# Optimization experiments

Hardware: AMD Instinct MI355X
Metric: run time of the kernel (lower is better)

## Reference

```python
import jax, jax.numpy as jnp
import numpy as np

B, N = 32, 256
PHI1, PHI2 = 64, 128
RHO1, RHO2, OUT = 256, 128, 64


def setup_inputs() -> dict:
    key = jax.random.key(0)
    ks = jax.random.split(key, 12)
    dm = jax.random.normal(ks[0], (B, N, N), dtype=jnp.float32)
    lengths = jnp.clip(jax.random.randint(ks[1], (B,), 0, N), 2, N).astype(jnp.int32)

    def lin(k, fan_in, fan_out):
        # torch nn.Linear default init: U(-1/sqrt(fan_in), 1/sqrt(fan_in))
        bound = 1.0 / np.sqrt(fan_in)
        kw, kb = jax.random.split(k)
        W = jax.random.uniform(kw, (fan_in, fan_out), jnp.float32, -bound, bound)
        b = jax.random.uniform(kb, (fan_out,), jnp.float32, -bound, bound)
        return W, b

    W1, b1 = lin(ks[2], 1, PHI1)
    W2, b2 = lin(ks[3], PHI1, PHI2)
    W3, b3 = lin(ks[4], PHI2, RHO1)
    W4, b4 = lin(ks[5], RHO1, RHO2)
    W5, b5 = lin(ks[6], RHO2, OUT)
    return {"dm": dm, "lengths": lengths, "W1": W1, "b1": b1, "W2": W2, "b2": b2,
            "W3": W3, "b3": b3, "W4": W4, "b4": b4, "W5": W5, "b5": b5}


def reference(dm, lengths, W1, b1, W2, b2, W3, b3, W4, b4, W5, b5):
    # Static upper-triangular (offset=1) index pairs: P = N*(N-1)/2
    iu0, iu1 = jnp.triu_indices(N, k=1)
    scalars = dm[:, iu0, iu1]                                   # [B, P]
    # Ragged mask: a pair (i, j) exists only if both indices < item length
    mask = (iu0[None, :] < lengths[:, None]) & (iu1[None, :] < lengths[:, None])  # [B, P]
    # phi MLP applied per scalar: 1 -> 64 -> 128, ReLU after each
    h = jax.nn.relu(scalars[..., None] * W1[0] + b1)            # [B, P, 64]
    h = jax.nn.relu(jnp.einsum('bpd,de->bpe', h, W2) + b2)      # [B, P, 128]
    # Masked sum-pool over pairs
    pooled = jnp.sum(h * mask[..., None].astype(h.dtype), axis=1)  # [B, 128]
    # rho MLP: 128 -> 256 -> 128 -> OUT (ReLU on hidden layers only)
    r = jax.nn.relu(pooled @ W3 + b3)
    r = jax.nn.relu(r @ W4 + b4)
    return r @ W5 + b5                                           # [B, OUT]
```

## Files before the change

### kernel.cpp

```cpp
#include <hip/hip_runtime.h>
#include <hip/hip_bf16.h>


#define NB 32
#define NN 256
#define PHI2 128
#define SEGS 65

__global__ __launch_bounds__(128) void build_tables(
    const float* __restrict__ W1, const float* __restrict__ b1,
    const float* __restrict__ W2, const float* __restrict__ b2,
    float2* __restrict__ table2,
    float* __restrict__ tsort, float* __restrict__ pooled) {
  __shared__ float w2_s[64 * PHI2];
  __shared__ float t_s[64], w1_s[64], b1_s[64];
  __shared__ int cat_s[64], rank_s[64];
  const int tid = threadIdx.x;
  const int seg = blockIdx.x;
  const float4* W2v = (const float4*)W2;
  float4* w2v = (float4*)w2_s;
  for (int i = tid; i < 64 * PHI2 / 4; i += 128) w2v[i] = W2v[i];
  if (tid < 64) {
    float w = W1[tid], bb = b1[tid];
    w1_s[tid] = w; b1_s[tid] = bb;
    int cat; float t;
    if (w > 0.f)      { cat = 0; t = -bb / w; }
    else if (w < 0.f) { cat = 1; t = -bb / w; }
    else              { cat = (bb > 0.f) ? 2 : 3; t = 0.f; }
    t_s[tid] = t; cat_s[tid] = cat;
  }
  __syncthreads();
  if (tid < 64) {
    float t = t_s[tid]; int r = 0;
    for (int k = 0; k < 64; ++k) {
      float tk = t_s[k];
      r += (tk < t) || (tk == t && k < tid);
    }
    rank_s[tid] = r;
    if (seg == 0) tsort[r] = t;
  }
  __syncthreads();
  float a = 0.f, bsum = b2[tid];
#pragma unroll 8
  for (int j = 0; j < 64; ++j) {
    int cat = cat_s[j], r = rank_s[j];
    bool act = (cat == 0) ? (seg > r) : (cat == 1) ? (seg <= r) : (cat == 2);
    float w2 = w2_s[j * PHI2 + tid];
    float m = act ? 1.f : 0.f;
    a    = fmaf(m * w1_s[j], w2, a);
    bsum = fmaf(m * b1_s[j], w2, bsum);
  }
  table2[seg * PHI2 + tid] = make_float2(a, bsum);
  if (seg == 0) {
    for (int i = tid; i < NB * PHI2; i += 128) pooled[i] = 0.f;
  }
}

__global__ __launch_bounds__(256) void phi_pool(
    const float* __restrict__ dm, const int* __restrict__ lengths,
    const float2* __restrict__ table2, const float* __restrict__ tsort,
    float* __restrict__ pooled) {
  __shared__ float2 ab_s[SEGS * PHI2];
  __shared__ float red_s[4][PHI2];
  const int chunk = blockIdx.x;
  const int b     = blockIdx.y;
  const int tid = threadIdx.x;
  const int lane = tid & 63, w = tid >> 6;

  const int len = lengths[b];
  if (chunk * 4 >= len - 1) return;

  for (int i = tid; i < SEGS * PHI2; i += 256) ab_s[i] = table2[i];
  __syncthreads();

  const float tv = tsort[lane];
  const float* dmb = dm + (size_t)b * (NN * NN);
  float acc0 = 0.f, acc1 = 0.f;

  for (int i0 = chunk * 4 + w; i0 < len - 1; i0 += 128) {
    const float* row = dmb + i0 * NN + i0 + 1;
    const int cnt_total = len - 1 - i0;
    for (int base = 0; base < cnt_total; base += 64) {
      const int cnt = min(64, cnt_total - base);
      float sv = (lane < cnt) ? row[base + lane] : 0.f;
      if (cnt == 64) {
#pragma unroll 8
        for (int j = 0; j < 64; ++j) {
          float s = __int_as_float(__builtin_amdgcn_readlane(__float_as_int(sv), j));
          int pos = (int)__popcll(__ballot(tv < s));
          const float2* rowp = ab_s + pos * PHI2;
          float2 p0 = rowp[lane];
          float2 p1 = rowp[64 + lane];
          acc0 += fmaxf(fmaf(p0.x, s, p0.y), 0.f);
          acc1 += fmaxf(fmaf(p1.x, s, p1.y), 0.f);
        }
      } else {
        for (int j = 0; j < cnt; ++j) {
          float s = __int_as_float(__builtin_amdgcn_readlane(__float_as_int(sv), j));
          int pos = (int)__popcll(__ballot(tv < s));
          const float2* rowp = ab_s + pos * PHI2;
          float2 p0 = rowp[lane];
          float2 p1 = rowp[64 + lane];
          acc0 += fmaxf(fmaf(p0.x, s, p0.y), 0.f);
          acc1 += fmaxf(fmaf(p1.x, s, p1.y), 0.f);
        }
      }
    }
  }
  red_s[w][lane] = acc0;
  red_s[w][64 + lane] = acc1;
  __syncthreads();
  if (tid < PHI2) {
    float v = red_s[0][tid] + red_s[1][tid] + red_s[2][tid] + red_s[3][tid];
    atomicAdd(&pooled[b * PHI2 + tid], v);
  }
}

__global__ __launch_bounds__(256) void rho_mlp(
    const float* __restrict__ pooled,
    const float* __restrict__ W3, const float* __restrict__ b3,
    const float* __restrict__ W4, const float* __restrict__ b4,
    const float* __restrict__ W5, const float* __restrict__ b5,
    float* __restrict__ out) {
  __shared__ float w_s[128 * 256];
  __shared__ float p_s[128], r1_s[256], r2_s[128];
  const int b = blockIdx.x, tid = threadIdx.x;
  float4* wsv = (float4*)w_s;
  {
    const float4* w3v = (const float4*)W3;
    for (int i = tid; i < 8192; i += 256) wsv[i] = w3v[i];
  }
  if (tid < 128) p_s[tid] = pooled[b * 128 + tid];
  __syncthreads();
  {
    float acc = b3[tid];
#pragma unroll 8
    for (int k = 0; k < 128; ++k) acc = fmaf(p_s[k], w_s[k * 256 + tid], acc);
    r1_s[tid] = fmaxf(acc, 0.f);
  }
  __syncthreads();
  {
    const float4* w4v = (const float4*)W4;
    for (int i = tid; i < 8192; i += 256) wsv[i] = w4v[i];
  }
  __syncthreads();
  if (tid < 128) {
    float acc = b4[tid];
#pragma unroll 8
    for (int k = 0; k < 256; ++k) acc = fmaf(r1_s[k], w_s[k * 128 + tid], acc);
    r2_s[tid] = fmaxf(acc, 0.f);
  }
  __syncthreads();
  {
    const float4* w5v = (const float4*)W5;
    for (int i = tid; i < 2048; i += 256) wsv[i] = w5v[i];
  }
  __syncthreads();
  if (tid < 64) {
    float acc = b5[tid];
#pragma unroll 8
    for (int k = 0; k < 128; ++k) acc = fmaf(r2_s[k], w_s[k * 64 + tid], acc);
    out[b * 64 + tid] = acc;
  }
}

extern "C" void kernel_launch(void* const* d_in, const int* in_sizes, int n_in,
                              void* d_out, int out_size, void* d_ws, size_t ws_size,
                              hipStream_t stream) {
  const float* dm      = (const float*)d_in[0];
  const int*   lengths = (const int*)d_in[1];
  const float* W1 = (const float*)d_in[2];
  const float* b1 = (const float*)d_in[3];
  const float* W2 = (const float*)d_in[4];
  const float* b2 = (const float*)d_in[5];
  const float* W3 = (const float*)d_in[6];
  const float* b3 = (const float*)d_in[7];
  const float* W4 = (const float*)d_in[8];
  const float* b4 = (const float*)d_in[9];
  const float* W5 = (const float*)d_in[10];
  const float* b5 = (const float*)d_in[11];

  float* ws = (float*)d_ws;
  float2* table2 = (float2*)ws;
  float* tsort   = ws + 16640;
  float* pooled  = ws + 16704;

  build_tables<<<SEGS, 128, 0, stream>>>(W1, b1, W2, b2, table2, tsort, pooled);
  phi_pool<<<dim3(32, NB), 256, 0, stream>>>(dm, lengths, table2, tsort, pooled);
  rho_mlp<<<NB, 256, 0, stream>>>(pooled, W3, b3, W4, b4, W5, b5, (float*)d_out);
}
```

Measured before the change: 157.4 us.

## Interleave phi table as float4, prefetch rows, use 512-thread blocks with direct atomics

The build_tables kernel now writes each segment's coefficients as float4 (a,b for channels lane and lane+64), so phi_pool fetches both channels with one 16-byte LDS read per pair instead of two float2 reads. phi_pool also loads the next 64-element chunk of the distance row before processing the current one, to hide global latency. Blocks grow to 8 waves (half as many chunks), which halves the per-block table copies into LDS. The shared-memory reduction is replaced by per-wave atomicAdds, which raises atomic traffic to pooled.

```diff
diff --git a/kernel.cpp b/kernel.cpp
--- a/kernel.cpp
+++ b/kernel.cpp
@@ -10,10 +10,11 @@
 __global__ __launch_bounds__(128) void build_tables(
     const float* __restrict__ W1, const float* __restrict__ b1,
     const float* __restrict__ W2, const float* __restrict__ b2,
-    float2* __restrict__ table2,
+    float4* __restrict__ table4,
     float* __restrict__ tsort, float* __restrict__ pooled) {
   __shared__ float w2_s[64 * PHI2];
   __shared__ float t_s[64], w1_s[64], b1_s[64];
+  __shared__ float a_sh[128], b_sh[128];
   __shared__ int cat_s[64], rank_s[64];
   const int tid = threadIdx.x;
   const int seg = blockIdx.x;
@@ -50,70 +51,68 @@
     a    = fmaf(m * w1_s[j], w2, a);
     bsum = fmaf(m * b1_s[j], w2, bsum);
   }
-  table2[seg * PHI2 + tid] = make_float2(a, bsum);
+  a_sh[tid] = a; b_sh[tid] = bsum;
+  __syncthreads();
+  if (tid < 64)
+    table4[seg * 64 + tid] =
+        make_float4(a_sh[tid], b_sh[tid], a_sh[tid + 64], b_sh[tid + 64]);
   if (seg == 0) {
     for (int i = tid; i < NB * PHI2; i += 128) pooled[i] = 0.f;
   }
 }
 
-__global__ __launch_bounds__(256) void phi_pool(
+__global__ __launch_bounds__(512) void phi_pool(
     const float* __restrict__ dm, const int* __restrict__ lengths,
-    const float2* __restrict__ table2, const float* __restrict__ tsort,
+    const float4* __restrict__ table4, const float* __restrict__ tsort,
     float* __restrict__ pooled) {
-  __shared__ float2 ab_s[SEGS * PHI2];
-  __shared__ float red_s[4][PHI2];
+  __shared__ float4 ab_s[SEGS * 64];
   const int chunk = blockIdx.x;
   const int b     = blockIdx.y;
   const int tid = threadIdx.x;
   const int lane = tid & 63, w = tid >> 6;
 
   const int len = lengths[b];
-  if (chunk * 4 >= len - 1) return;
+  if (chunk * 8 >= len - 1) return;
 
-  for (int i = tid; i < SEGS * PHI2; i += 256) ab_s[i] = table2[i];
+  for (int i = tid; i < SEGS * 64; i += 512) ab_s[i] = table4[i];
   __syncthreads();
 
   const float tv = tsort[lane];
   const float* dmb = dm + (size_t)b * (NN * NN);
   float acc0 = 0.f, acc1 = 0.f;
 
-  for (int i0 = chunk * 4 + w; i0 < len - 1; i0 += 128) {
+  for (int i0 = chunk * 8 + w; i0 < len - 1; i0 += 128) {
     const float* row = dmb + i0 * NN + i0 + 1;
     const int cnt_total = len - 1 - i0;
+    float sv = (lane < cnt_total) ? row[lane] : 0.f;
     for (int base = 0; base < cnt_total; base += 64) {
       const int cnt = min(64, cnt_total - base);
-      float sv = (lane < cnt) ? row[base + lane] : 0.f;
+      const int nb = base + 64;
+      float svn = 0.f;
+      if (nb < cnt_total && lane < cnt_total - nb) svn = row[nb + lane];
       if (cnt == 64) {
 #pragma unroll 8
         for (int j = 0; j < 64; ++j) {
           float s = __int_as_float(__builtin_amdgcn_readlane(__float_as_int(sv), j));
           int pos = (int)__popcll(__ballot(tv < s));
-          const float2* rowp = ab_s + pos * PHI2;
-          float2 p0 = rowp[lane];
-          float2 p1 = rowp[64 + lane];
-          acc0 += fmaxf(fmaf(p0.x, s, p0.y), 0.f);
-          acc1 += fmaxf(fmaf(p1.x, s, p1.y), 0.f);
+          float4 p = ab_s[pos * 64 + lane];
+          acc0 += fmaxf(fmaf(p.x, s, p.y), 0.f);
+          acc1 += fmaxf(fmaf(p.z, s, p.w), 0.f);
         }
       } else {
         for (int j = 0; j < cnt; ++j) {
           float s = __int_as_float(__builtin_amdgcn_readlane(__float_as_int(sv), j));
           int pos = (int)__popcll(__ballot(tv < s));
-          const float2* rowp = ab_s + pos * PHI2;
-          float2 p0 = rowp[lane];
-          float2 p1 = rowp[64 + lane];
-          acc0 += fmaxf(fmaf(p0.x, s, p0.y), 0.f);
-          acc1 += fmaxf(fmaf(p1.x, s, p1.y), 0.f);
+          float4 p = ab_s[pos * 64 + lane];
+          acc0 += fmaxf(fmaf(p.x, s, p.y), 0.f);
+          acc1 += fmaxf(fmaf(p.z, s, p.w), 0.f);
         }
       }
+      sv = svn;
     }
   }
-  red_s[w][lane] = acc0;
-  red_s[w][64 + lane] = acc1;
-  __syncthreads();
-  if (tid < PHI2) {
-    float v = red_s[0][tid] + red_s[1][tid] + red_s[2][tid] + red_s[3][tid];
-    atomicAdd(&pooled[b * PHI2 + tid], v);
-  }
+  atomicAdd(&pooled[b * PHI2 + lane], acc0);
+  atomicAdd(&pooled[b * PHI2 + 64 + lane], acc1);
 }
 
 __global__ __launch_bounds__(256) void rho_mlp(
@@ -181,11 +180,11 @@
   const float* b5 = (const float*)d_in[11];
 
   float* ws = (float*)d_ws;
-  float2* table2 = (float2*)ws;
+  float4* table4 = (float4*)ws;
   float* tsort   = ws + 16640;
   float* pooled  = ws + 16704;
 
-  build_tables<<<SEGS, 128, 0, stream>>>(W1, b1, W2, b2, table2, tsort, pooled);
-  phi_pool<<<dim3(32, NB), 256, 0, stream>>>(dm, lengths, table2, tsort, pooled);
+  build_tables<<<SEGS, 128, 0, stream>>>(W1, b1, W2, b2, table4, tsort, pooled);
+  phi_pool<<<dim3(16, NB), 512, 0, stream>>>(dm, lengths, table4, tsort, pooled);
   rho_mlp<<<NB, 256, 0, stream>>>(pooled, W3, b3, W4, b4, W5, b5, (float*)d_out);
 }
```

Result: faster. 142.9 us (-9.2%).
